# Performance work log

Measured on AMD Instinct MI355X. Metric: run time of the kernel, lower is better.

## Reference

```python
import jax, jax.numpy as jnp
import numpy as np

B = 4096        # graphs per batch
N_PER = 64      # nodes per graph
N = B * N_PER   # total nodes
D = 512         # embed_dim
T = 2048        # target_size


def setup_inputs() -> dict:
    key = jax.random.key(0)
    k1, k2, k3 = jax.random.split(key, 3)
    batch_emb = jax.random.normal(k1, (N, D), dtype=jnp.float32)
    # sorted per-node graph ids (PyG `batch` vector), all graphs non-empty
    seg = jnp.repeat(jnp.arange(B, dtype=jnp.int64), N_PER)
    # local node indices of the two query nodes in each graph
    targets = jax.random.randint(k2, (B, 2), 0, N_PER, dtype=jnp.int64)
    W = jax.random.normal(k3, (T, 3 * D), dtype=jnp.float32) * (1.0 / np.sqrt(3 * D))
    b = jnp.zeros((T,), dtype=jnp.float32)
    return {"batch_emb": batch_emb, "seg": seg, "targets": targets, "W": W, "b": b}


def reference(batch_emb, seg, targets, W, b):
    # per-graph mean pooling (segment mean)
    sums = jax.ops.segment_sum(batch_emb, seg, num_segments=B)          # [B, D]
    counts = jax.ops.segment_sum(jnp.ones((batch_emb.shape[0],), batch_emb.dtype),
                                 seg, num_segments=B)                   # [B]
    node_avg = sums / counts[:, None]                                   # [B, D]
    # convert local query indices to global node indices via segment starts
    starts = jnp.cumsum(counts.astype(jnp.int64)) - counts.astype(jnp.int64)  # [B]
    global_idx = starts[:, None] + targets                              # [B, 2]
    q = batch_emb[global_idx]                                           # [B, 2, D]
    final_embs = jnp.concatenate([q[:, 0], q[:, 1], node_avg], axis=-1) # [B, 3D]
    return final_embs @ W.T + b                                         # [B, T]
```

## Files before the change

### kernel.cpp

```cpp
#include <hip/hip_runtime.h>
#include <hip/hip_bf16.h>
#include <stdint.h>

#define B_GRAPHS 4096
#define N_PER    64
#define D_EMB    512
#define T_OUT    2048
#define K_DIM    1536
#define KT_N     24
#define WCONV_BLOCKS 512

typedef __bf16 bf16x8 __attribute__((ext_vector_type(8)));
typedef float  f32x4  __attribute__((ext_vector_type(4)));

__global__ __launch_bounds__(128) void pool_conv_kernel(
    const float* __restrict__ emb, const int* __restrict__ targets,
    const float* __restrict__ W,
    __hip_bfloat16* __restrict__ lhs, __hip_bfloat16* __restrict__ wb)
{
    union Pack { __hip_bfloat16 h[4]; uint2 u; };

    if (blockIdx.x >= B_GRAPHS) {
        const int total = T_OUT * K_DIM / 4;
        const int nthr  = WCONV_BLOCKS * 128;
        for (int i = (blockIdx.x - B_GRAPHS) * 128 + threadIdx.x;
             i < total; i += nthr) {
            const float4 v = reinterpret_cast<const float4*>(W)[i];
            Pack p;
            p.h[0] = __float2bfloat16(v.x); p.h[1] = __float2bfloat16(v.y);
            p.h[2] = __float2bfloat16(v.z); p.h[3] = __float2bfloat16(v.w);
            reinterpret_cast<uint2*>(wb)[i] = p.u;
        }
        return;
    }

    const int g = blockIdx.x;
    const int t = threadIdx.x;
    const int t0 = targets[2*g];
    const int t1 = targets[2*g + 1];
    const float4* rows = reinterpret_cast<const float4*>(emb)
                         + (size_t)g * N_PER * (D_EMB/4) + t;
    float4 acc = make_float4(0.f, 0.f, 0.f, 0.f);
    #pragma unroll 16
    for (int n = 0; n < N_PER; ++n) {
        float4 v = rows[(size_t)n * (D_EMB/4)];
        acc.x += v.x; acc.y += v.y; acc.z += v.z; acc.w += v.w;
    }
    const float s = 1.0f / (float)N_PER;
    float4 avg = make_float4(acc.x*s, acc.y*s, acc.z*s, acc.w*s);
    float4 q0 = rows[(size_t)t0 * (D_EMB/4)];
    float4 q1 = rows[(size_t)t1 * (D_EMB/4)];

    __hip_bfloat16* row = lhs + (size_t)g * K_DIM;
    Pack p0, p1, pa;
    p0.h[0] = __float2bfloat16(q0.x); p0.h[1] = __float2bfloat16(q0.y);
    p0.h[2] = __float2bfloat16(q0.z); p0.h[3] = __float2bfloat16(q0.w);
    p1.h[0] = __float2bfloat16(q1.x); p1.h[1] = __float2bfloat16(q1.y);
    p1.h[2] = __float2bfloat16(q1.z); p1.h[3] = __float2bfloat16(q1.w);
    pa.h[0] = __float2bfloat16(avg.x); pa.h[1] = __float2bfloat16(avg.y);
    pa.h[2] = __float2bfloat16(avg.z); pa.h[3] = __float2bfloat16(avg.w);
    reinterpret_cast<uint2*>(row)[t]             = p0.u;
    reinterpret_cast<uint2*>(row + D_EMB)[t]     = p1.u;
    reinterpret_cast<uint2*>(row + 2*D_EMB)[t]   = pa.u;
}

__global__ __launch_bounds__(256) void gemm_kernel(
    const __hip_bfloat16* __restrict__ A,
    const __hip_bfloat16* __restrict__ Bm,
    const float* __restrict__ bias,
    float* __restrict__ C)
{
    __shared__ __align__(16) __hip_bfloat16 As[128*64];
    __shared__ __align__(16) __hip_bfloat16 Bs[128*64];

    const int tid = threadIdx.x;
    const int w   = tid >> 6;
    const int l   = tid & 63;
    const int wr  = w >> 1;
    const int wc  = w & 1;
    const int brow = blockIdx.y * 128;
    const int bcol = blockIdx.x * 128;

    const int sr   = l >> 3;
    const int scol = 8 * ((l & 7) ^ sr);

    char* AsB = reinterpret_cast<char*>(As);
    char* BsB = reinterpret_cast<char*>(Bs);

    f32x4 acc[4][4];
    #pragma unroll
    for (int m = 0; m < 4; ++m)
        #pragma unroll
        for (int n = 0; n < 4; ++n)
            acc[m][n] = (f32x4){0.f, 0.f, 0.f, 0.f};

    for (int kt = 0; kt < KT_N; ++kt) {
        const int k0 = kt * 64;
        if (kt) __syncthreads();
        #pragma unroll
        for (int c = 0; c < 4; ++c) {
            const int ch = w * 4 + c;
            const int r  = ch * 8 + sr;
            const __hip_bfloat16* ga = A  + (size_t)(brow + r) * K_DIM + k0 + scol;
            const __hip_bfloat16* gb = Bm + (size_t)(bcol + r) * K_DIM + k0 + scol;
            __builtin_amdgcn_global_load_lds(
                (const __attribute__((address_space(1))) void*)ga,
                (__attribute__((address_space(3))) void*)(AsB + ch*1024), 16, 0, 0);
            __builtin_amdgcn_global_load_lds(
                (const __attribute__((address_space(1))) void*)gb,
                (__attribute__((address_space(3))) void*)(BsB + ch*1024), 16, 0, 0);
        }
        __syncthreads();

        #pragma unroll
        for (int kk = 0; kk < 2; ++kk) {
            const int kbyte = kk*64 + (l >> 4)*16;
            bf16x8 af[4], bf[4];
            #pragma unroll
            for (int m = 0; m < 4; ++m) {
                const int r = wr*64 + m*16 + (l & 15);
                af[m] = *reinterpret_cast<const bf16x8*>(
                            AsB + r*128 + (kbyte ^ ((r & 7) << 4)));
            }
            #pragma unroll
            for (int n = 0; n < 4; ++n) {
                const int r = wc*64 + n*16 + (l & 15);
                bf[n] = *reinterpret_cast<const bf16x8*>(
                            BsB + r*128 + (kbyte ^ ((r & 7) << 4)));
            }
            #pragma unroll
            for (int m = 0; m < 4; ++m)
                #pragma unroll
                for (int n = 0; n < 4; ++n)
                    acc[m][n] = __builtin_amdgcn_mfma_f32_16x16x32_bf16(
                                    af[m], bf[n], acc[m][n], 0, 0, 0);
        }
    }

    #pragma unroll
    for (int n = 0; n < 4; ++n) {
        const int col = bcol + wc*64 + n*16 + (l & 15);
        const float bv = bias[col];
        #pragma unroll
        for (int m = 0; m < 4; ++m) {
            const int row0 = brow + wr*64 + m*16 + (l >> 4)*4;
            #pragma unroll
            for (int e = 0; e < 4; ++e) {
                __builtin_nontemporal_store(acc[m][n][e] + bv,
                    &C[(size_t)(row0 + e) * T_OUT + col]);
            }
        }
    }
}

extern "C" void kernel_launch(void* const* d_in, const int* in_sizes, int n_in,
                              void* d_out, int out_size, void* d_ws, size_t ws_size,
                              hipStream_t stream) {
    const float* emb     = (const float*)d_in[0];
    const int*   targets = (const int*)d_in[2];
    const float* W       = (const float*)d_in[3];
    const float* bias    = (const float*)d_in[4];
    float* out = (float*)d_out;

    __hip_bfloat16* lhs = (__hip_bfloat16*)d_ws;
    __hip_bfloat16* wb  = lhs + (size_t)B_GRAPHS * K_DIM;

    pool_conv_kernel<<<B_GRAPHS + WCONV_BLOCKS, 128, 0, stream>>>(
        emb, targets, W, lhs, wb);
    gemm_kernel<<<dim3(T_OUT/128, B_GRAPHS/128), 256, 0, stream>>>(lhs, wb, bias, out);
}
```

Baseline: 144.9 us.

## Triple-buffer GEMM with 128x256 tiles and asynchronous LDS staging

Restructures the bf16 GEMM into a 3-stage LDS ring with BK=32 and prefetch two tiles ahead. It uses manual vmcnt waits and a single barrier per iteration, so global loads overlap MFMA work. The block tile grows to 128x256 for more reuse per LDS fetch, and occupancy is hinted at 2 blocks per CU. The XOR swizzle on LDS reads is dropped, which risks bank conflicts, and the larger tile increases register pressure.

```diff
diff --git a/kernel.cpp b/kernel.cpp
--- a/kernel.cpp
+++ b/kernel.cpp
@@ -7,8 +7,13 @@
 #define D_EMB    512
 #define T_OUT    2048
 #define K_DIM    1536
-#define KT_N     24
 #define WCONV_BLOCKS 512
+
+#define BM   128
+#define BN   256
+#define BK   32
+#define KT_N (K_DIM/BK)
+#define NBUF 3
 
 typedef __bf16 bf16x8 __attribute__((ext_vector_type(8)));
 typedef float  f32x4  __attribute__((ext_vector_type(4)));
@@ -64,82 +69,94 @@
     reinterpret_cast<uint2*>(row + 2*D_EMB)[t]   = pa.u;
 }
 
-__global__ __launch_bounds__(256) void gemm_kernel(
+__global__ __launch_bounds__(256, 2) void gemm_kernel(
     const __hip_bfloat16* __restrict__ A,
     const __hip_bfloat16* __restrict__ Bm,
     const float* __restrict__ bias,
     float* __restrict__ C)
 {
-    __shared__ __align__(16) __hip_bfloat16 As[128*64];
-    __shared__ __align__(16) __hip_bfloat16 Bs[128*64];
+    __shared__ __align__(16) __hip_bfloat16 As[NBUF][BM*BK];
+    __shared__ __align__(16) __hip_bfloat16 Bs[NBUF][BN*BK];
 
-    const int tid = threadIdx.x;
-    const int w   = tid >> 6;
-    const int l   = tid & 63;
-    const int wr  = w >> 1;
-    const int wc  = w & 1;
-    const int brow = blockIdx.y * 128;
-    const int bcol = blockIdx.x * 128;
+    const int t  = threadIdx.x;
+    const int w  = t >> 6;
+    const int l  = t & 63;
+    const int wr = w >> 1;
+    const int wc = w & 1;
+    const int brow = blockIdx.y * BM;
+    const int bcol = blockIdx.x * BN;
 
-    const int sr   = l >> 3;
-    const int scol = 8 * ((l & 7) ^ sr);
+    const int srow = l >> 2;
+    const int scol = (l & 3) * 8;
 
-    char* AsB = reinterpret_cast<char*>(As);
-    char* BsB = reinterpret_cast<char*>(Bs);
-
-    f32x4 acc[4][4];
+    f32x4 acc[4][8];
     #pragma unroll
     for (int m = 0; m < 4; ++m)
         #pragma unroll
-        for (int n = 0; n < 4; ++n)
+        for (int n = 0; n < 8; ++n)
             acc[m][n] = (f32x4){0.f, 0.f, 0.f, 0.f};
 
-    for (int kt = 0; kt < KT_N; ++kt) {
-        const int k0 = kt * 64;
-        if (kt) __syncthreads();
+    auto stage = [&](int b, int kt) {
+        const int k0 = kt * BK;
+        char* Ab = reinterpret_cast<char*>(As[b]);
+        char* Bb = reinterpret_cast<char*>(Bs[b]);
+        #pragma unroll
+        for (int c = 0; c < 2; ++c) {
+            const int ch = w * 2 + c;
+            const __hip_bfloat16* ga =
+                A + (size_t)(brow + ch*16 + srow) * K_DIM + k0 + scol;
+            __builtin_amdgcn_global_load_lds(
+                (const __attribute__((address_space(1))) void*)ga,
+                (__attribute__((address_space(3))) void*)(Ab + ch*1024), 16, 0, 0);
+        }
         #pragma unroll
         for (int c = 0; c < 4; ++c) {
             const int ch = w * 4 + c;
-            const int r  = ch * 8 + sr;
-            const __hip_bfloat16* ga = A  + (size_t)(brow + r) * K_DIM + k0 + scol;
-            const __hip_bfloat16* gb = Bm + (size_t)(bcol + r) * K_DIM + k0 + scol;
-            __builtin_amdgcn_global_load_lds(
-                (const __attribute__((address_space(1))) void*)ga,
-                (__attribute__((address_space(3))) void*)(AsB + ch*1024), 16, 0, 0);
+            const __hip_bfloat16* gb =
+                Bm + (size_t)(bcol + ch*16 + srow) * K_DIM + k0 + scol;
             __builtin_amdgcn_global_load_lds(
                 (const __attribute__((address_space(1))) void*)gb,
-                (__attribute__((address_space(3))) void*)(BsB + ch*1024), 16, 0, 0);
+                (__attribute__((address_space(3))) void*)(Bb + ch*1024), 16, 0, 0);
         }
-        __syncthreads();
+    };
 
+    stage(0, 0);
+    stage(1, 1);
+
+    const int kb = (l >> 4) * 16;
+
+    for (int kt = 0; kt < KT_N; ++kt) {
+        if (kt + 1 < KT_N) asm volatile("s_waitcnt vmcnt(6)" ::: "memory");
+        else               asm volatile("s_waitcnt vmcnt(0)" ::: "memory");
+        __builtin_amdgcn_s_barrier();
+
+        if (kt + 2 < KT_N) stage((kt + 2) % NBUF, kt + 2);
+
+        const char* Ab = reinterpret_cast<const char*>(As[kt % NBUF]);
+        const char* Bb = reinterpret_cast<const char*>(Bs[kt % NBUF]);
+
+        bf16x8 af[4], bf[8];
         #pragma unroll
-        for (int kk = 0; kk < 2; ++kk) {
-            const int kbyte = kk*64 + (l >> 4)*16;
-            bf16x8 af[4], bf[4];
+        for (int m = 0; m < 4; ++m) {
+            const int r = wr*64 + m*16 + (l & 15);
+            af[m] = *reinterpret_cast<const bf16x8*>(Ab + r*64 + kb);
+        }
+        #pragma unroll
+        for (int n = 0; n < 8; ++n) {
+            const int r = wc*128 + n*16 + (l & 15);
+            bf[n] = *reinterpret_cast<const bf16x8*>(Bb + r*64 + kb);
+        }
+        #pragma unroll
+        for (int m = 0; m < 4; ++m)
             #pragma unroll
-            for (int m = 0; m < 4; ++m) {
-                const int r = wr*64 + m*16 + (l & 15);
-                af[m] = *reinterpret_cast<const bf16x8*>(
-                            AsB + r*128 + (kbyte ^ ((r & 7) << 4)));
-            }
-            #pragma unroll
-            for (int n = 0; n < 4; ++n) {
-                const int r = wc*64 + n*16 + (l & 15);
-                bf[n] = *reinterpret_cast<const bf16x8*>(
-                            BsB + r*128 + (kbyte ^ ((r & 7) << 4)));
-            }
-            #pragma unroll
-            for (int m = 0; m < 4; ++m)
-                #pragma unroll
-                for (int n = 0; n < 4; ++n)
-                    acc[m][n] = __builtin_amdgcn_mfma_f32_16x16x32_bf16(
-                                    af[m], bf[n], acc[m][n], 0, 0, 0);
-        }
+            for (int n = 0; n < 8; ++n)
+                acc[m][n] = __builtin_amdgcn_mfma_f32_16x16x32_bf16(
+                                af[m], bf[n], acc[m][n], 0, 0, 0);
     }
 
     #pragma unroll
-    for (int n = 0; n < 4; ++n) {
-        const int col = bcol + wc*64 + n*16 + (l & 15);
+    for (int n = 0; n < 8; ++n) {
+        const int col = bcol + wc*128 + n*16 + (l & 15);
         const float bv = bias[col];
         #pragma unroll
         for (int m = 0; m < 4; ++m) {
@@ -167,5 +184,5 @@
 
     pool_conv_kernel<<<B_GRAPHS + WCONV_BLOCKS, 128, 0, stream>>>(
         emb, targets, W, lhs, wb);
-    gemm_kernel<<<dim3(T_OUT/128, B_GRAPHS/128), 256, 0, stream>>>(lhs, wb, bias, out);
+    gemm_kernel<<<dim3(T_OUT/BN, B_GRAPHS/BM), 256, 0, stream>>>(lhs, wb, bias, out);
 }
```

Result: slower. 175.9 us (+21.4%).
